# Performance work log

Measured on AMD Instinct MI355X. Metric: run time of the kernel, lower is better.

Reference implementation:

```python
import jax, jax.numpy as jnp
import numpy as np

NUM_CLASSES = 100
NUM_PROTOS = 10
FEAT_DIM = 1024
BATCH = 16384
NALL = NUM_CLASSES * NUM_PROTOS


def setup_inputs() -> dict:
    key = jax.random.key(0)
    k1, k2, k3 = jax.random.split(key, 3)
    x = jax.random.normal(k1, (BATCH, FEAT_DIM), dtype=jnp.float32)
    protos = jax.random.normal(k2, (NALL, FEAT_DIM), dtype=jnp.float32)
    enc_w = jax.random.normal(k3, (FEAT_DIM, FEAT_DIM), dtype=jnp.float32) / np.sqrt(FEAT_DIM)
    enc_b = jnp.zeros((FEAT_DIM,), dtype=jnp.float32)
    return {"x": x, "protos": protos, "enc_w": enc_w, "enc_b": enc_b}


def reference(x, protos, enc_w, enc_b):
    # encoder(protos): linear projection, (nall, F)
    ep = protos @ enc_w + enc_b
    # Pairwise euclidean distance via GEMM-based squared-distance trick:
    x_sq = jnp.sum(x * x, axis=-1, keepdims=True)            # (B, 1)
    p_sq = jnp.sum(ep * ep, axis=-1)                          # (nall,)
    d2 = x_sq - 2.0 * (x @ ep.T) + p_sq[None, :]              # (B, nall)
    d = jnp.sqrt(jnp.maximum(d2, 0.0))                        # L2 norm, clamp fp error
    # reshape matches torch: index = proto * num_classes + class
    d = d.reshape(x.shape[0], NUM_PROTOS, NUM_CLASSES)
    return jnp.min(d, axis=1)                                 # (B, num_classes)
```

## Files before the change

### kernel.cpp

```cpp
#include <hip/hip_runtime.h>
#include <hip/hip_bf16.h>
#include <stdint.h>

#define FEAT 1024
#define NALL 1000
#define NPAD 1120
#define NCLS 100

typedef __attribute__((ext_vector_type(8))) short short8;
typedef __attribute__((ext_vector_type(4))) float f32x4;
typedef __attribute__((ext_vector_type(4))) unsigned short us4;

__device__ __forceinline__ unsigned short f2bf(float f) {
    union { float f; uint32_t u; } v; v.f = f;
    uint32_t u = v.u;
    return (unsigned short)((u + 0x7FFFu + ((u >> 16) & 1u)) >> 16);
}

__device__ __forceinline__ void gload16(const void* g, void* l) {
    __builtin_amdgcn_global_load_lds((__attribute__((address_space(1))) void*)g,
                                     (__attribute__((address_space(3))) void*)l,
                                     16, 0, 0);
}

__global__ __launch_bounds__(256) void k_prep_x(const float* __restrict__ x,
                                                unsigned short* __restrict__ xb,
                                                float* __restrict__ xsq) {
    int row = blockIdx.x * 4 + (threadIdx.x >> 6);
    int lane = threadIdx.x & 63;
    const float4* xr = (const float4*)(x + (size_t)row * FEAT);
    float s = 0.f;
#pragma unroll
    for (int i = 0; i < 4; ++i) {
        float4 v = xr[lane + i * 64];
        s += v.x * v.x + v.y * v.y + v.z * v.z + v.w * v.w;
        us4 o;
        o[0] = f2bf(v.x); o[1] = f2bf(v.y); o[2] = f2bf(v.z); o[3] = f2bf(v.w);
        *(us4*)(xb + (size_t)row * FEAT + (size_t)(lane + i * 64) * 4) = o;
    }
#pragma unroll
    for (int off = 32; off; off >>= 1) s += __shfl_xor(s, off);
    if (lane == 0) xsq[row] = s;
}

__global__ __launch_bounds__(256) void k_prep_protos(const float* __restrict__ p,
                                                     unsigned short* __restrict__ pb) {
    int row = blockIdx.x;
    int t = threadIdx.x;
    us4 o;
    if (row < NALL) {
        float4 v = ((const float4*)(p + (size_t)row * FEAT))[t];
        o[0] = f2bf(v.x); o[1] = f2bf(v.y); o[2] = f2bf(v.z); o[3] = f2bf(v.w);
    } else {
        o[0] = 0; o[1] = 0; o[2] = 0; o[3] = 0;
    }
    *(us4*)(pb + (size_t)row * FEAT + (size_t)t * 4) = o;
}

__global__ __launch_bounds__(256) void k_transpose_w(const float* __restrict__ w,
                                                     unsigned short* __restrict__ wt) {
    __shared__ float tile[32][33];
    int bx = blockIdx.x, by = blockIdx.y;
    int tx = threadIdx.x & 31, ty = threadIdx.x >> 5;
#pragma unroll
    for (int i = 0; i < 4; ++i) {
        int r = by * 32 + ty + i * 8;
        tile[ty + i * 8][tx] = w[(size_t)r * FEAT + bx * 32 + tx];
    }
    __syncthreads();
#pragma unroll
    for (int i = 0; i < 4; ++i) {
        int r = bx * 32 + ty + i * 8;
        wt[(size_t)r * FEAT + by * 32 + tx] = f2bf(tile[tx][ty + i * 8]);
    }
}

__global__ __launch_bounds__(256) void k_enc_gemm(const unsigned short* __restrict__ A,
                                                  const unsigned short* __restrict__ B,
                                                  const float* __restrict__ bias,
                                                  unsigned short* __restrict__ epb) {
    __shared__ __align__(16) char smem[32768];
    int bm0 = (blockIdx.x >> 3) * 128;
    int bn0 = (blockIdx.x & 7) * 128;
    int tid = threadIdx.x, lane = tid & 63, wid = tid >> 6;
    int wm = wid >> 1, wn = wid & 1;
    int ls = lane >> 4, lf = lane & 15;
    f32x4 acc[4][4] = {};
    for (int k0 = 0; k0 < FEAT; k0 += 64) {
        __syncthreads();
#pragma unroll
        for (int i = 0; i < 4; ++i) {
            int ci = wid + i * 4;
            int r = ci * 8 + (lane >> 3), c = (lane & 7) * 8;
            gload16(A + (size_t)(bm0 + r) * FEAT + k0 + c, smem + ci * 1024);
            gload16(B + (size_t)(bn0 + r) * FEAT + k0 + c, smem + 16384 + ci * 1024);
        }
        __syncthreads();
#pragma unroll
        for (int kk = 0; kk < 64; kk += 32) {
            short8 a[4], b[4];
#pragma unroll
            for (int f = 0; f < 4; ++f) {
                a[f] = *(const short8*)(smem + (wm * 64 + f * 16 + lf) * 128 + (kk + ls * 8) * 2);
                b[f] = *(const short8*)(smem + 16384 + (wn * 64 + f * 16 + lf) * 128 + (kk + ls * 8) * 2);
            }
#pragma unroll
            for (int fm = 0; fm < 4; ++fm)
#pragma unroll
                for (int fn = 0; fn < 4; ++fn)
                    acc[fm][fn] = __builtin_amdgcn_mfma_f32_16x16x32_bf16(a[fm], b[fn], acc[fm][fn], 0, 0, 0);
        }
    }
    int tr = ls * 4, tc = lf;
#pragma unroll
    for (int fn = 0; fn < 4; ++fn) {
        int col = bn0 + wn * 64 + fn * 16 + tc;
        float bb = bias[col];
#pragma unroll
        for (int fm = 0; fm < 4; ++fm) {
#pragma unroll
            for (int r = 0; r < 4; ++r) {
                int row = bm0 + wm * 64 + fm * 16 + tr + r;
                if (row < NALL) {
                    int pr = (row % 100) * 10 + row / 100;
                    epb[(size_t)pr * FEAT + col] = f2bf(acc[fm][fn][r] + bb);
                }
            }
        }
    }
}

__global__ __launch_bounds__(256) void k_psq(const unsigned short* __restrict__ epb,
                                             float* __restrict__ psq) {
    int row = blockIdx.x * 4 + (threadIdx.x >> 6);
    int lane = threadIdx.x & 63;
    if (row >= NPAD) return;
    float s = 0.f;
    const short8* r8 = (const short8*)(epb + (size_t)row * FEAT);
#pragma unroll
    for (int i = 0; i < 2; ++i) {
        short8 v = r8[lane + i * 64];
#pragma unroll
        for (int j = 0; j < 8; ++j) {
            union { uint32_t u; float f; } c;
            c.u = ((uint32_t)(unsigned short)v[j]) << 16;
            s += c.f * c.f;
        }
    }
#pragma unroll
    for (int off = 32; off; off >>= 1) s += __shfl_xor(s, off);
    if (lane == 0) psq[row] = (row < NALL) ? s : 1e30f;
}

__global__ __launch_bounds__(256, 4) void k_main(const unsigned short* __restrict__ xb,
                                                 const unsigned short* __restrict__ epb,
                                                 const float* __restrict__ xsq,
                                                 const float* __restrict__ psq,
                                                 float* __restrict__ out) {
    __shared__ __align__(16) char smem[27648];
    const int bid = blockIdx.x;
    const int swz = (bid & 7) * 224 + (bid >> 3);
    const int bm0 = (swz / 14) * 128;
    const int nt  = swz % 14;
    const int bn0 = nt * 80;
    const int tid = threadIdx.x, lane = tid & 63, wid = tid >> 6;
    const int ls = lane >> 4, lf = lane & 15;
    float* xsq_s = (float*)(smem + 26624);
    float* psq_s = (float*)(smem + 27136);
    if (tid < 128) xsq_s[tid] = xsq[bm0 + tid];
    if (tid < 80)  psq_s[tid] = psq[bn0 + tid];

    const int sr = lane >> 3, scb = lane & 7;
    const int scol = ((scb ^ sr) << 3);
    const unsigned short* aptr[4];
    const unsigned short* bptr[3];
#pragma unroll
    for (int i = 0; i < 4; ++i)
        aptr[i] = xb + (size_t)(bm0 + (wid + i * 4) * 8 + sr) * FEAT + scol;
#pragma unroll
    for (int j = 0; j < 3; ++j) {
        int cj = wid + j * 4;
        bptr[j] = epb + (size_t)(bn0 + (cj < 10 ? cj : 0) * 8 + sr) * FEAT + scol;
    }

    int raA[2], raB[5];
#pragma unroll
    for (int f = 0; f < 2; ++f) raA[f] = (wid * 32 + f * 16 + lf) * 128;
#pragma unroll
    for (int f = 0; f < 5; ++f) raB[f] = 16384 + (f * 16 + lf) * 128;
    const int sw = lf & 7;

    f32x4 acc[2][5] = {};

    for (int t = 0; t < 16; ++t) {
        __syncthreads();
#pragma unroll
        for (int i = 0; i < 4; ++i)
            gload16(aptr[i], smem + (wid + i * 4) * 1024);
#pragma unroll
        for (int j = 0; j < 3; ++j) {
            int cj = wid + j * 4;
            if (cj < 10) gload16(bptr[j], smem + 16384 + cj * 1024);
        }
#pragma unroll
        for (int i = 0; i < 4; ++i) aptr[i] += 64;
#pragma unroll
        for (int j = 0; j < 3; ++j) bptr[j] += 64;
        __syncthreads();
#pragma unroll
        for (int kk2 = 0; kk2 < 2; ++kk2) {
            const int off = (((kk2 * 4 + ls) ^ sw) << 4);
            short8 a[2], b[5];
#pragma unroll
            for (int f = 0; f < 2; ++f)
                a[f] = *(const short8*)(smem + raA[f] + off);
#pragma unroll
            for (int f = 0; f < 5; ++f)
                b[f] = *(const short8*)(smem + raB[f] + off);
#pragma unroll
            for (int fm = 0; fm < 2; ++fm)
#pragma unroll
                for (int fn = 0; fn < 5; ++fn)
                    acc[fm][fn] = __builtin_amdgcn_mfma_f32_16x16x32_bf16(a[fm], b[fn], acc[fm][fn], 0, 0, 0);
        }
    }

    float* dls = (float*)smem;
    const int tr = ls * 4;
#pragma unroll
    for (int p = 0; p < 2; ++p) {
        __syncthreads();
#pragma unroll
        for (int fn = 0; fn < 5; ++fn) {
            int col = fn * 16 + lf;
            float pq = psq_s[col];
#pragma unroll
            for (int r = 0; r < 4; ++r) {
                float d2 = xsq_s[wid * 32 + p * 16 + tr + r] - 2.f * acc[p][fn][r] + pq;
                dls[(wid * 16 + tr + r) * 81 + col] = sqrtf(fmaxf(d2, 0.f));
            }
        }
        __syncthreads();
#pragma unroll
        for (int i = 0; i < 2; ++i) {
            int task = tid + i * 256;
            int rr = task >> 3, cl = task & 7;
            float m = 1e30f;
#pragma unroll
            for (int j = 0; j < 10; ++j) m = fminf(m, dls[rr * 81 + cl * 10 + j]);
            int grow = bm0 + (rr >> 4) * 32 + p * 16 + (rr & 15);
            int gcls = nt * 8 + cl;
            if (gcls < NCLS) out[(size_t)grow * NCLS + gcls] = m;
        }
    }
}

extern "C" void kernel_launch(void* const* d_in, const int* in_sizes, int n_in,
                              void* d_out, int out_size, void* d_ws, size_t ws_size,
                              hipStream_t stream) {
    const float* x      = (const float*)d_in[0];
    const float* protos = (const float*)d_in[1];
    const float* enc_w  = (const float*)d_in[2];
    const float* enc_b  = (const float*)d_in[3];
    float* out = (float*)d_out;
    char* ws = (char*)d_ws;

    unsigned short* xb  = (unsigned short*)ws;
    unsigned short* epb = (unsigned short*)(ws + 33554432);
    unsigned short* prb = (unsigned short*)(ws + 35848192);
    unsigned short* wtb = (unsigned short*)(ws + 37945344);
    float* xsq = (float*)(ws + 40042496);
    float* psq = (float*)(ws + 40108032);

    hipMemsetAsync(epb + (size_t)1000 * FEAT, 0, (size_t)120 * FEAT * 2, stream);

    k_prep_x<<<4096, 256, 0, stream>>>(x, xb, xsq);
    k_prep_protos<<<1024, 256, 0, stream>>>(protos, prb);
    k_transpose_w<<<dim3(32, 32), 256, 0, stream>>>(enc_w, wtb);
    k_enc_gemm<<<64, 256, 0, stream>>>(prb, wtb, enc_b, epb);
    k_psq<<<280, 256, 0, stream>>>(epb, psq);
    k_main<<<1792, 256, 0, stream>>>(xb, epb, xsq, psq, out);
}
```

Baseline: 109.1 us.

## Fuse proto conversion and norm into encoder GEMM, trim main grid padding

The proto fp32-to-bf16 conversion moves into the encoder GEMM's shared-memory load, and the squared norms of the encoded protos are computed in its epilogue with shuffles and atomics. This removes the k_prep_protos and k_psq launches and the padded proto buffer. The main kernel now uses 13 column tiles instead of 14, with the last tile overlapping at columns 920-999 so the padded proto rows are never read. The trade-offs are that norms come from fp32 values rather than bf16-rounded ones, and the overlapping tile rewrites a few output classes.

```diff
diff --git a/kernel.cpp b/kernel.cpp
--- a/kernel.cpp
+++ b/kernel.cpp
@@ -4,7 +4,6 @@
 
 #define FEAT 1024
 #define NALL 1000
-#define NPAD 1120
 #define NCLS 100
 
 typedef __attribute__((ext_vector_type(8))) short short8;
@@ -43,20 +42,6 @@
     if (lane == 0) xsq[row] = s;
 }
 
-__global__ __launch_bounds__(256) void k_prep_protos(const float* __restrict__ p,
-                                                     unsigned short* __restrict__ pb) {
-    int row = blockIdx.x;
-    int t = threadIdx.x;
-    us4 o;
-    if (row < NALL) {
-        float4 v = ((const float4*)(p + (size_t)row * FEAT))[t];
-        o[0] = f2bf(v.x); o[1] = f2bf(v.y); o[2] = f2bf(v.z); o[3] = f2bf(v.w);
-    } else {
-        o[0] = 0; o[1] = 0; o[2] = 0; o[3] = 0;
-    }
-    *(us4*)(pb + (size_t)row * FEAT + (size_t)t * 4) = o;
-}
-
 __global__ __launch_bounds__(256) void k_transpose_w(const float* __restrict__ w,
                                                      unsigned short* __restrict__ wt) {
     __shared__ float tile[32][33];
@@ -75,24 +60,38 @@
     }
 }
 
-__global__ __launch_bounds__(256) void k_enc_gemm(const unsigned short* __restrict__ A,
-                                                  const unsigned short* __restrict__ B,
-                                                  const float* __restrict__ bias,
-                                                  unsigned short* __restrict__ epb) {
+__global__ __launch_bounds__(256) void k_enc(const float* __restrict__ protos,
+                                             const unsigned short* __restrict__ B,
+                                             const float* __restrict__ bias,
+                                             unsigned short* __restrict__ epb,
+                                             float* __restrict__ psq) {
     __shared__ __align__(16) char smem[32768];
     int bm0 = (blockIdx.x >> 3) * 128;
     int bn0 = (blockIdx.x & 7) * 128;
     int tid = threadIdx.x, lane = tid & 63, wid = tid >> 6;
     int wm = wid >> 1, wn = wid & 1;
     int ls = lane >> 4, lf = lane & 15;
+
+    const int er = tid >> 1;
+    const bool ev = (bm0 + er) < NALL;
+    const float* ap = protos + (size_t)(bm0 + er) * FEAT + (tid & 1) * 32;
+    us4* ad = (us4*)smem + er * 16 + (tid & 1) * 8;
+
     f32x4 acc[4][4] = {};
     for (int k0 = 0; k0 < FEAT; k0 += 64) {
         __syncthreads();
+#pragma unroll
+        for (int i = 0; i < 8; ++i) {
+            float4 v = ev ? *(const float4*)(ap + k0 + i * 4)
+                          : make_float4(0.f, 0.f, 0.f, 0.f);
+            us4 o;
+            o[0] = f2bf(v.x); o[1] = f2bf(v.y); o[2] = f2bf(v.z); o[3] = f2bf(v.w);
+            ad[i] = o;
+        }
 #pragma unroll
         for (int i = 0; i < 4; ++i) {
             int ci = wid + i * 4;
             int r = ci * 8 + (lane >> 3), c = (lane & 7) * 8;
-            gload16(A + (size_t)(bm0 + r) * FEAT + k0 + c, smem + ci * 1024);
             gload16(B + (size_t)(bn0 + r) * FEAT + k0 + c, smem + 16384 + ci * 1024);
         }
         __syncthreads();
@@ -112,6 +111,7 @@
         }
     }
     int tr = ls * 4, tc = lf;
+    float sq[4][4] = {};
 #pragma unroll
     for (int fn = 0; fn < 4; ++fn) {
         int col = bn0 + wn * 64 + fn * 16 + tc;
@@ -121,35 +121,28 @@
 #pragma unroll
             for (int r = 0; r < 4; ++r) {
                 int row = bm0 + wm * 64 + fm * 16 + tr + r;
+                float v = acc[fm][fn][r] + bb;
+                sq[fm][r] += v * v;
                 if (row < NALL) {
                     int pr = (row % 100) * 10 + row / 100;
-                    epb[(size_t)pr * FEAT + col] = f2bf(acc[fm][fn][r] + bb);
+                    epb[(size_t)pr * FEAT + col] = f2bf(v);
                 }
             }
         }
     }
-}
-
-__global__ __launch_bounds__(256) void k_psq(const unsigned short* __restrict__ epb,
-                                             float* __restrict__ psq) {
-    int row = blockIdx.x * 4 + (threadIdx.x >> 6);
-    int lane = threadIdx.x & 63;
-    if (row >= NPAD) return;
-    float s = 0.f;
-    const short8* r8 = (const short8*)(epb + (size_t)row * FEAT);
-#pragma unroll
-    for (int i = 0; i < 2; ++i) {
-        short8 v = r8[lane + i * 64];
-#pragma unroll
-        for (int j = 0; j < 8; ++j) {
-            union { uint32_t u; float f; } c;
-            c.u = ((uint32_t)(unsigned short)v[j]) << 16;
-            s += c.f * c.f;
-        }
-    }
-#pragma unroll
-    for (int off = 32; off; off >>= 1) s += __shfl_xor(s, off);
-    if (lane == 0) psq[row] = (row < NALL) ? s : 1e30f;
+#pragma unroll
+    for (int fm = 0; fm < 4; ++fm)
+#pragma unroll
+        for (int r = 0; r < 4; ++r) {
+            float s = sq[fm][r];
+            s += __shfl_xor(s, 1); s += __shfl_xor(s, 2);
+            s += __shfl_xor(s, 4); s += __shfl_xor(s, 8);
+            int row = bm0 + wm * 64 + fm * 16 + tr + r;
+            if (lf == 0 && row < NALL) {
+                int pr = (row % 100) * 10 + row / 100;
+                atomicAdd(psq + pr, s);
+            }
+        }
 }
 
 __global__ __launch_bounds__(256, 4) void k_main(const unsigned short* __restrict__ xb,
@@ -159,10 +152,11 @@
                                                  float* __restrict__ out) {
     __shared__ __align__(16) char smem[27648];
     const int bid = blockIdx.x;
-    const int swz = (bid & 7) * 224 + (bid >> 3);
-    const int bm0 = (swz / 14) * 128;
-    const int nt  = swz % 14;
-    const int bn0 = nt * 80;
+    const int swz = (bid & 7) * 208 + (bid >> 3);
+    const int bm0 = (swz / 13) * 128;
+    const int nt  = swz % 13;
+    const int bn0 = (nt < 12) ? nt * 80 : 920;
+    const int cls0 = (nt < 12) ? nt * 8 : 92;
     const int tid = threadIdx.x, lane = tid & 63, wid = tid >> 6;
     const int ls = lane >> 4, lf = lane & 15;
     float* xsq_s = (float*)(smem + 26624);
@@ -249,8 +243,7 @@
 #pragma unroll
             for (int j = 0; j < 10; ++j) m = fminf(m, dls[rr * 81 + cl * 10 + j]);
             int grow = bm0 + (rr >> 4) * 32 + p * 16 + (rr & 15);
-            int gcls = nt * 8 + cl;
-            if (gcls < NCLS) out[(size_t)grow * NCLS + gcls] = m;
+            out[(size_t)grow * NCLS + cls0 + cl] = m;
         }
     }
 }
@@ -267,17 +260,14 @@
 
     unsigned short* xb  = (unsigned short*)ws;
     unsigned short* epb = (unsigned short*)(ws + 33554432);
-    unsigned short* prb = (unsigned short*)(ws + 35848192);
-    unsigned short* wtb = (unsigned short*)(ws + 37945344);
-    float* xsq = (float*)(ws + 40042496);
-    float* psq = (float*)(ws + 40108032);
-
-    hipMemsetAsync(epb + (size_t)1000 * FEAT, 0, (size_t)120 * FEAT * 2, stream);
+    unsigned short* wtb = (unsigned short*)(ws + 35848192);
+    float* xsq = (float*)(ws + 37945344);
+    float* psq = (float*)(ws + 38010880);
+
+    hipMemsetAsync(psq, 0, (size_t)NALL * 4, stream);
 
     k_prep_x<<<4096, 256, 0, stream>>>(x, xb, xsq);
-    k_prep_protos<<<1024, 256, 0, stream>>>(protos, prb);
     k_transpose_w<<<dim3(32, 32), 256, 0, stream>>>(enc_w, wtb);
-    k_enc_gemm<<<64, 256, 0, stream>>>(prb, wtb, enc_b, epb);
-    k_psq<<<280, 256, 0, stream>>>(epb, psq);
-    k_main<<<1792, 256, 0, stream>>>(xb, epb, xsq, psq, out);
-}
+    k_enc<<<64, 256, 0, stream>>>(protos, wtb, enc_b, epb, psq);
+    k_main<<<1664, 256, 0, stream>>>(xb, epb, xsq, psq, out);
+}
```

New measurement: 120.7 us. 10.7% more time.
